# Kernel tuning notes

Hardware: AMD Instinct MI355X
Metric: run time of the kernel (lower is better)

Reference implementation:

```python
import jax, jax.numpy as jnp
import numpy as np

N_NODES = 20000
N_EDGES = 320000
IN_CH = 64
OUT_CH = 128

def _gat(x, src, dst, W, a_src, a_dst, bias, concat):
    # PyG GATConv: linear -> per-edge leaky_relu attention logits -> segment softmax over dst -> scatter-weighted sum
    N = x.shape[0]
    H, C = a_src.shape
    xl = (x @ W).reshape(N, H, C)                       # [N,H,C]
    al = (xl * a_src).sum(-1)                           # [N,H] src logits
    ar = (xl * a_dst).sum(-1)                           # [N,H] dst logits
    e = jax.nn.leaky_relu(al[src] + ar[dst], 0.2)       # [E,H]
    emax = jax.ops.segment_max(e, dst, num_segments=N)  # every node has a self loop -> no empty segments
    ee = jnp.exp(e - emax[dst])
    denom = jax.ops.segment_sum(ee, dst, num_segments=N)
    alpha = ee / (denom[dst] + 1e-16)                   # [E,H]
    out = jax.ops.segment_sum(xl[src] * alpha[:, :, None], dst, num_segments=N)  # [N,H,C]
    out = out.reshape(N, H * C) if concat else out.mean(axis=1)
    return out + bias

def setup_inputs() -> dict:
    key = jax.random.key(0)
    ks = jax.random.split(key, 32)
    def lin(k, fi, fo):
        return jax.random.normal(k, (fi, fo), jnp.float32) / np.sqrt(fi)
    def att(k, H, C):
        return jax.random.normal(k, (H, C), jnp.float32) / np.sqrt(C)
    x = jax.random.normal(ks[0], (N_NODES, IN_CH), jnp.float32)
    src = jax.random.randint(ks[1], (N_EDGES,), 0, N_NODES, jnp.int32)
    dst = jax.random.randint(ks[2], (N_EDGES,), 0, N_NODES, jnp.int32)
    dst = jnp.where(dst == src, (dst + 1) % N_NODES, dst)  # avoid pre-existing self loops
    edge_index = jnp.stack([src, dst])
    edge_time = jax.random.uniform(ks[3], (N_EDGES,), jnp.float32)
    H = 4
    return {
        "x": x, "edge_time": edge_time,
        "W1": lin(ks[4], IN_CH, 512), "as1": att(ks[5], H, 128), "ad1": att(ks[6], H, 128), "b1": jnp.zeros((512,), jnp.float32),
        "W2": lin(ks[7], 512, 512),   "as2": att(ks[8], H, 128), "ad2": att(ks[9], H, 128), "b2": jnp.zeros((512,), jnp.float32),
        "W3": lin(ks[10], 512, 512),  "as3": att(ks[11], H, 128), "ad3": att(ks[12], H, 128), "b3": jnp.zeros((OUT_CH,), jnp.float32),
        "tW1": lin(ks[13], 1, 64), "tb1": jnp.zeros((64,), jnp.float32),
        "tW2": lin(ks[14], 64, OUT_CH), "tb2": jnp.zeros((OUT_CH,), jnp.float32),
        "fW1": lin(ks[15], 2 * OUT_CH, OUT_CH), "fb1": jnp.zeros((OUT_CH,), jnp.float32),
        "fW2": lin(ks[16], OUT_CH, OUT_CH), "fb2": jnp.zeros((OUT_CH,), jnp.float32),
        "ln_g": jnp.ones((OUT_CH,), jnp.float32), "ln_b": jnp.zeros((OUT_CH,), jnp.float32),
        "rW": lin(ks[17], IN_CH, OUT_CH), "rb": jnp.zeros((OUT_CH,), jnp.float32),
        "edge_index": edge_index,
    }

def reference(x, edge_time, W1, as1, ad1, b1, W2, as2, ad2, b2, W3, as3, ad3, b3,
              tW1, tb1, tW2, tb2, fW1, fb1, fW2, fb2, ln_g, ln_b, rW, rb, edge_index):
    N = x.shape[0]
    loop = jnp.arange(N, dtype=edge_index.dtype)
    src = jnp.concatenate([edge_index[0], loop])
    dst = jnp.concatenate([edge_index[1], loop])
    # temporal embedding of raw (pre-self-loop) edges
    t = edge_time[:, None]
    time_emb = jax.nn.relu(t @ tW1 + tb1) @ tW2 + tb2    # [E, OUT_CH]
    x_res = x @ rW + rb
    h = jax.nn.relu(_gat(x, src, dst, W1, as1, ad1, b1, True))
    h = jax.nn.relu(_gat(h, src, dst, W2, as2, ad2, b2, True))
    h = jax.nn.relu(_gat(h, src, dst, W3, as3, ad3, b3, False))
    # x_agg[row] += h[col]  with (row, col) = (src, dst) incl. self loops
    agg = jax.ops.segment_sum(h[dst], src, num_segments=N)
    tm = jnp.broadcast_to(time_emb.mean(axis=0)[None, :], (N, time_emb.shape[1]))
    z = jnp.concatenate([agg, tm], axis=1)
    z = jax.nn.relu(z @ fW1 + fb1)                        # dropout is identity in eval
    z = z @ fW2 + fb2
    mu = z.mean(-1, keepdims=True)
    var = ((z - mu) ** 2).mean(-1, keepdims=True)
    z = (z - mu) / jnp.sqrt(var + 1e-5) * ln_g + ln_b
    return z + x_res
```

## Files before the change

### kernel.cpp

```cpp
#include <hip/hip_runtime.h>
#include <hip/hip_bf16.h>
#include <math.h>

typedef short bf16x8 __attribute__((ext_vector_type(8)));
typedef float f32x4 __attribute__((ext_vector_type(4)));

__device__ __forceinline__ float lrelu(float v) { return v > 0.f ? v : 0.2f * v; }

__device__ __forceinline__ void gload16(const void* g, void* l) {
  __builtin_amdgcn_global_load_lds(
      (const __attribute__((address_space(1))) void*)g,
      (__attribute__((address_space(3))) void*)l, 16, 0, 0);
}

__device__ __forceinline__ uint packbf(float v0, float v1) {
  __hip_bfloat16 h0 = __float2bfloat16(v0);
  __hip_bfloat16 h1 = __float2bfloat16(v1);
  return (uint)(*(unsigned short*)&h0) | ((uint)(*(unsigned short*)&h1) << 16);
}

__global__ void k_count(const int* __restrict__ src, const int* __restrict__ dst, int E,
                        int* cntD, int* cntS) {
  int e = blockIdx.x * blockDim.x + threadIdx.x;
  if (e < E) {
    atomicAdd(&cntD[dst[e]], 1);
    atomicAdd(&cntS[src[e]], 1);
  }
}

__global__ __launch_bounds__(1024) void k_scan2(const int* __restrict__ cntD, int* __restrict__ offD,
                                                const int* __restrict__ cntS, int* __restrict__ offS,
                                                int n) {
  const int* cnt = blockIdx.x ? cntS : cntD;
  int* off = blockIdx.x ? offS : offD;
  __shared__ int sums[1024];
  int t = threadIdx.x;
  int PT = (n + 1023) >> 10;
  int start = t * PT;
  int local = 0;
  for (int i = 0; i < PT; ++i) {
    int idx = start + i;
    if (idx < n) local += cnt[idx];
  }
  sums[t] = local;
  __syncthreads();
  for (int o = 1; o < 1024; o <<= 1) {
    int v = (t >= o) ? sums[t - o] : 0;
    __syncthreads();
    sums[t] += v;
    __syncthreads();
  }
  int run = sums[t] - local;
  for (int i = 0; i < PT; ++i) {
    int idx = start + i;
    if (idx < n) { off[idx] = run; run += cnt[idx]; }
  }
  if (t == 1023) off[n] = run;
}

__global__ void k_fill(const int* __restrict__ src, const int* __restrict__ dst, int E,
                       const int* __restrict__ offD, int* curD, int* lstD,
                       const int* __restrict__ offS, int* curS, int* lstS) {
  int e = blockIdx.x * blockDim.x + threadIdx.x;
  if (e < E) {
    int d = dst[e], s = src[e];
    int p = atomicAdd(&curD[d], 1);
    lstD[offD[d] + p] = s;
    int q = atomicAdd(&curS[s], 1);
    lstS[offS[s] + q] = d;
  }
}

__global__ __launch_bounds__(256) void k_time_reduce(const float* __restrict__ et,
    const float* __restrict__ tW1, const float* __restrict__ tb1,
    float* __restrict__ tacc, int E) {
  __shared__ float se[256];
  __shared__ float buf[256];
  int t = threadIdx.x;
  int l = t & 63, w = t >> 6;
  float wk = tW1[l], bk = tb1[l];
  float a0 = 0.f, a1 = 0.f, a2 = 0.f, a3 = 0.f;
  for (int base = blockIdx.x * 256; base < E; base += gridDim.x * 256) {
    int idx = base + t;
    se[t] = (idx < E) ? et[idx] : 0.f;
    __syncthreads();
    int cnt = E - base; if (cnt > 256) cnt = 256;
    int s0 = w * 64;
    int c = cnt - s0; if (c < 0) c = 0; if (c > 64) c = 64;
    int j = 0;
    for (; j + 4 <= c; j += 4) {
      float v0 = se[s0 + j], v1 = se[s0 + j + 1];
      float v2 = se[s0 + j + 2], v3 = se[s0 + j + 3];
      a0 += fmaxf(v0 * wk + bk, 0.f);
      a1 += fmaxf(v1 * wk + bk, 0.f);
      a2 += fmaxf(v2 * wk + bk, 0.f);
      a3 += fmaxf(v3 * wk + bk, 0.f);
    }
    for (; j < c; ++j) a0 += fmaxf(se[s0 + j] * wk + bk, 0.f);
    __syncthreads();
  }
  buf[t] = (a0 + a1) + (a2 + a3);
  __syncthreads();
  if (t < 64) {
    float s = buf[t] + buf[t + 64] + buf[t + 128] + buf[t + 192];
    atomicAdd(&tacc[t], s);
  }
}

__global__ __launch_bounds__(128) void k_time_combine(const float* __restrict__ tacc,
    const float* __restrict__ tW2, const float* __restrict__ tb2,
    const float* __restrict__ fW1, const float* __restrict__ fb1,
    float* __restrict__ cvec, int E) {
  __shared__ float tm[128];
  int t = threadIdx.x;
  float inv = 1.f / (float)E;
  float acc = tb2[t];
  for (int k = 0; k < 64; ++k) acc += (tacc[k] * inv) * tW2[k * 128 + t];
  tm[t] = acc;
  __syncthreads();
  float c = fb1[t];
  for (int k = 0; k < 128; ++k) c += tm[k] * fW1[(128 + k) * 128 + t];
  cvec[t] = c;
}

struct PrepArgs {
  const float* W[6]; __hip_bfloat16* Wt[6]; int K[6]; int Nw[6]; int tstart[6];
  int NC, XB;
};

__global__ __launch_bounds__(256) void k_prep(PrepArgs a, const float* __restrict__ x,
    __hip_bfloat16* __restrict__ xbf, __hip_bfloat16* __restrict__ habf,
    __hip_bfloat16* __restrict__ aggbf, int N, int Mp) {
  __shared__ float tile[32][65];
  int bid = blockIdx.x;
  int t = threadIdx.x;
  if (bid < a.NC) {
    int m = 0;
#pragma unroll
    for (int i = 1; i < 6; ++i) if (bid >= a.tstart[i]) m = i;
    const float* W = a.W[m];
    __hip_bfloat16* Wt = a.Wt[m];
    int K = a.K[m], Nw = a.Nw[m];
    int lt = bid - a.tstart[m];
    int ntn = Nw >> 6;
    int bk = (lt / ntn) * 32, bn = (lt % ntn) * 64;
    int rn = t & 63, rk = t >> 6;
#pragma unroll
    for (int i = 0; i < 8; ++i)
      tile[rk + i * 4][rn] = W[(size_t)(bk + rk + i * 4) * Nw + bn + rn];
    __syncthreads();
    int wk2 = (t & 15) * 2, wn = t >> 4;
    uint* Wo = (uint*)Wt;
#pragma unroll
    for (int i = 0; i < 4; ++i) {
      int n = wn + i * 16;
      Wo[((size_t)(bn + n) * K + bk + wk2) >> 1] = packbf(tile[wk2][n], tile[wk2 + 1][n]);
    }
  } else if (bid < a.NC + a.XB) {
    int i4 = (bid - a.NC) * 256 + t;
    int row = i4 >> 4;
    float4 v = make_float4(0.f, 0.f, 0.f, 0.f);
    if (row < N) v = ((const float4*)x)[i4];
    uint2 p; p.x = packbf(v.x, v.y); p.y = packbf(v.z, v.w);
    ((uint2*)xbf)[i4] = p;
  } else {
    int row = N + (bid - a.NC - a.XB);
    ((uint*)habf)[(size_t)row * 256 + t] = 0;
    if (t < 64) ((uint*)aggbf)[(size_t)row * 64 + t] = 0;
  }
}

template<int EPI>
__global__ __launch_bounds__(256) void gemm_t(
    const __hip_bfloat16* __restrict__ A, const __hip_bfloat16* __restrict__ Bt,
    void* __restrict__ Cout, const float* __restrict__ bias,
    int M, int Nw, int K, int relu, int Nn,
    const float* __restrict__ asrc, const float* __restrict__ adst,
    float* __restrict__ al, float* __restrict__ ar,
    float* __restrict__ C2, const float* __restrict__ bias2,
    const float* __restrict__ lng, const float* __restrict__ lnb,
    float* __restrict__ resid)
{
  __shared__ short As[128 * 32];
  __shared__ short Bs[128 * 32];
  int tid = threadIdx.x;
  int bm = blockIdx.x * 128;
  int cb = blockIdx.y;
  int bn = cb * 128;
  int w = tid >> 6, l = tid & 63;
  int wr = (w >> 1) * 64, wc = (w & 1) * 64;
  f32x4 acc[4][4] = {};
  const short* Ag = (const short*)A;
  const short* Bg = (const short*)Bt;

  for (int k0 = 0; k0 < K; k0 += 32) {
#pragma unroll
    for (int i = 0; i < 2; ++i) {
      int slot = i * 256 + tid;
      int row = slot >> 2;
      int col = (slot & 3) * 8;
      gload16(Ag + (size_t)(bm + row) * K + k0 + col, &As[slot * 8]);
      gload16(Bg + (size_t)(bn + row) * K + k0 + col, &Bs[slot * 8]);
    }
    __syncthreads();
    bf16x8 af[4], bfr[4];
#pragma unroll
    for (int m = 0; m < 4; ++m)
      af[m] = *(const bf16x8*)&As[(wr + m * 16 + (l & 15)) * 32 + (l >> 4) * 8];
#pragma unroll
    for (int n = 0; n < 4; ++n)
      bfr[n] = *(const bf16x8*)&Bs[(wc + n * 16 + (l & 15)) * 32 + (l >> 4) * 8];
#pragma unroll
    for (int m = 0; m < 4; ++m)
#pragma unroll
      for (int n = 0; n < 4; ++n)
        acc[m][n] = __builtin_amdgcn_mfma_f32_16x16x32_bf16(af[m], bfr[n], acc[m][n], 0, 0, 0);
    __syncthreads();
  }

  int g = l >> 4, cc = l & 15, cr = g * 4;

  if (EPI == 0) {
#pragma unroll
    for (int n = 0; n < 4; ++n) {
      int col = bn + wc + n * 16 + cc;
      float bb = bias ? bias[col] : 0.f;
#pragma unroll
      for (int m = 0; m < 4; ++m) {
#pragma unroll
        for (int r = 0; r < 4; ++r) {
          int gm = bm + wr + m * 16 + cr + r;
          if (gm < M) {
            float v = acc[m][n][r] + bb;
            if (relu) v = fmaxf(v, 0.f);
            ((__hip_bfloat16*)Cout)[(size_t)gm * Nw + col] = __float2bfloat16(v);
          }
        }
      }
    }
  }

  if (EPI == 1) {
    if (cb < 4) {
#pragma unroll
      for (int n = 0; n < 4; ++n) {
        int col = bn + wc + n * 16 + cc;
#pragma unroll
        for (int m = 0; m < 4; ++m) {
#pragma unroll
          for (int r = 0; r < 4; ++r) {
            int gm = bm + wr + m * 16 + cr + r;
            if (gm < M)
              ((__hip_bfloat16*)Cout)[(size_t)gm * 512 + col] = __float2bfloat16(acc[m][n][r]);
          }
        }
      }
      float asv[4], adv[4];
#pragma unroll
      for (int n = 0; n < 4; ++n) {
        int ch = bn + wc + n * 16 + cc;
        asv[n] = asrc[ch]; adv[n] = adst[ch];
      }
      float* spal = (float*)As;
      float* spar = spal + 256;
#pragma unroll
      for (int m = 0; m < 4; ++m) {
#pragma unroll
        for (int r = 0; r < 4; ++r) {
          float pa = acc[m][0][r] * asv[0] + acc[m][1][r] * asv[1]
                   + acc[m][2][r] * asv[2] + acc[m][3][r] * asv[3];
          float pb = acc[m][0][r] * adv[0] + acc[m][1][r] * adv[1]
                   + acc[m][2][r] * adv[2] + acc[m][3][r] * adv[3];
#pragma unroll
          for (int o = 1; o < 16; o <<= 1) {
            pa += __shfl_xor(pa, o);
            pb += __shfl_xor(pb, o);
          }
          if (cc == 0) {
            int rl = m * 16 + cr + r;
            spal[w * 64 + rl] = pa;
            spar[w * 64 + rl] = pb;
          }
        }
      }
      __syncthreads();
      if ((w & 1) == 0) {
        float av = spal[w * 64 + l] + spal[(w + 1) * 64 + l];
        float rv = spar[w * 64 + l] + spar[(w + 1) * 64 + l];
        int row = bm + wr + l;
        if (row < Nn) { al[row * 4 + cb] = av; ar[row * 4 + cb] = rv; }
      }
    } else {
#pragma unroll
      for (int n = 0; n < 4; ++n) {
        int col2 = wc + n * 16 + cc;
        float bb = bias2[col2];
#pragma unroll
        for (int m = 0; m < 4; ++m) {
#pragma unroll
          for (int r = 0; r < 4; ++r) {
            int gm = bm + wr + m * 16 + cr + r;
            if (gm < Nn) C2[(size_t)gm * 128 + col2] = acc[m][n][r] + bb;
          }
        }
      }
    }
  }

  if (EPI == 2) {
    float bb[4], gl_[4], gb_[4];
#pragma unroll
    for (int n = 0; n < 4; ++n) {
      int col = wc + n * 16 + cc;
      bb[n] = bias[col]; gl_[n] = lng[col]; gb_[n] = lnb[col];
    }
    float* ssum = (float*)As;
    float* ssq = ssum + 256;
    float* smu = ssum + 512;
    float* srs = ssum + 640;
#pragma unroll
    for (int m = 0; m < 4; ++m) {
#pragma unroll
      for (int r = 0; r < 4; ++r) {
        float s = 0.f, q = 0.f;
#pragma unroll
        for (int n = 0; n < 4; ++n) {
          float z = acc[m][n][r] + bb[n];
          s += z; q += z * z;
        }
#pragma unroll
        for (int o = 1; o < 16; o <<= 1) {
          s += __shfl_xor(s, o);
          q += __shfl_xor(q, o);
        }
        if (cc == 0) {
          int rl = m * 16 + cr + r;
          ssum[w * 64 + rl] = s;
          ssq[w * 64 + rl] = q;
        }
      }
    }
    __syncthreads();
    if ((w & 1) == 0) {
      float s = ssum[w * 64 + l] + ssum[(w + 1) * 64 + l];
      float q = ssq[w * 64 + l] + ssq[(w + 1) * 64 + l];
      float mu = s * (1.f / 128.f);
      float var = q * (1.f / 128.f) - mu * mu;
      smu[wr + l] = mu;
      srs[wr + l] = rsqrtf(var + 1e-5f);
    }
    __syncthreads();
#pragma unroll
    for (int m = 0; m < 4; ++m) {
#pragma unroll
      for (int r = 0; r < 4; ++r) {
        int rl = wr + m * 16 + cr + r;
        int gm = bm + rl;
        if (gm < M) {
          float mu = smu[rl], rs = srs[rl];
#pragma unroll
          for (int n = 0; n < 4; ++n) {
            int col = wc + n * 16 + cc;
            float z = acc[m][n][r] + bb[n];
            float y = (z - mu) * rs * gl_[n] + gb_[n] + resid[(size_t)gm * 128 + col];
            resid[(size_t)gm * 128 + col] = y;
          }
        }
      }
    }
  }
}

__global__ __launch_bounds__(256) void k_gat_agg(
    const __hip_bfloat16* __restrict__ xl, const float* __restrict__ al,
    const float* __restrict__ ar, const int* __restrict__ off,
    const int* __restrict__ lst, const float* __restrict__ bias,
    __hip_bfloat16* __restrict__ outb, __hip_bfloat16* __restrict__ outh,
    int mode, int N)
{
  __shared__ int   sside[4][64];
  __shared__ float sebuf[4][4][68];
  int w = threadIdx.x >> 6, l = threadIdx.x & 63;
  int d = blockIdx.x * 4 + w;
  bool active = (d < N);
  int base = 0, deg = 0, tot = 0;
  float4 arv = make_float4(0.f, 0.f, 0.f, 0.f);
  if (active) {
    base = off[d]; deg = off[d + 1] - base; tot = deg + 1;
    arv = *(const float4*)(ar + 4 * d);
  }
  int hh = l >> 4;
  float facc[8] = {0.f, 0.f, 0.f, 0.f, 0.f, 0.f, 0.f, 0.f};
  float dn0 = 0.f, dn1 = 0.f, dn2 = 0.f, dn3 = 0.f;
  const uint4* xw = (const uint4*)xl;
  for (int cb = 0; cb < tot; cb += 64) {
    int j = cb + l;
    float e0 = 0.f, e1 = 0.f, e2 = 0.f, e3 = 0.f;
    int sid = 0;
    if (j < tot) {
      sid = (j == deg) ? d : lst[base + j];
      float4 av = *(const float4*)(al + 4 * sid);
      e0 = __expf(lrelu(av.x + arv.x));
      e1 = __expf(lrelu(av.y + arv.y));
      e2 = __expf(lrelu(av.z + arv.z));
      e3 = __expf(lrelu(av.w + arv.w));
      dn0 += e0; dn1 += e1; dn2 += e2; dn3 += e3;
    }
    sside[w][l] = sid;
    sebuf[w][0][l] = e0; sebuf[w][1][l] = e1;
    sebuf[w][2][l] = e2; sebuf[w][3][l] = e3;
    int cnt = tot - cb; if (cnt > 64) cnt = 64;
#pragma unroll 2
    for (int jj = 0; jj < cnt; ++jj) {
      int sid2 = sside[w][jj];
      float e = sebuf[w][hh][jj];
      uint4 pv = xw[(size_t)sid2 * 64 + l];
      facc[0] += e * __uint_as_float(pv.x << 16);
      facc[1] += e * __uint_as_float(pv.x & 0xffff0000u);
      facc[2] += e * __uint_as_float(pv.y << 16);
      facc[3] += e * __uint_as_float(pv.y & 0xffff0000u);
      facc[4] += e * __uint_as_float(pv.z << 16);
      facc[5] += e * __uint_as_float(pv.z & 0xffff0000u);
      facc[6] += e * __uint_as_float(pv.w << 16);
      facc[7] += e * __uint_as_float(pv.w & 0xffff0000u);
    }
  }
#pragma unroll
  for (int o = 1; o < 64; o <<= 1) {
    dn0 += __shfl_xor(dn0, o); dn1 += __shfl_xor(dn1, o);
    dn2 += __shfl_xor(dn2, o); dn3 += __shfl_xor(dn3, o);
  }
  if (!active) return;
  float dsel = hh == 0 ? dn0 : hh == 1 ? dn1 : hh == 2 ? dn2 : dn3;
  float rden = 1.f / dsel;
  if (mode == 0) {
    int c8 = l * 8;
    const float4* bp = (const float4*)(bias + c8);
    float4 b0 = bp[0], b1 = bp[1];
    float vb[8] = {b0.x, b0.y, b0.z, b0.w, b1.x, b1.y, b1.z, b1.w};
    uint4 o4; uint* po = (uint*)&o4;
#pragma unroll
    for (int i = 0; i < 4; ++i) {
      float v0 = fmaxf(facc[2*i]   * rden + vb[2*i],   0.f);
      float v1 = fmaxf(facc[2*i+1] * rden + vb[2*i+1], 0.f);
      po[i] = packbf(v0, v1);
    }
    ((uint4*)outb)[(size_t)d * 64 + l] = o4;
  } else {
#pragma unroll
    for (int i = 0; i < 8; ++i) {
      facc[i] *= rden;
      facc[i] += __shfl_xor(facc[i], 16);
      facc[i] += __shfl_xor(facc[i], 32);
    }
    if (l < 16) {
      int c = l * 8;
      const float4* bp = (const float4*)(bias + c);
      float4 b0 = bp[0], b1 = bp[1];
      float vb[8] = {b0.x, b0.y, b0.z, b0.w, b1.x, b1.y, b1.z, b1.w};
      uint4 o4; uint* po = (uint*)&o4;
#pragma unroll
      for (int i = 0; i < 4; ++i) {
        float v0 = fmaxf(facc[2*i]   * 0.25f + vb[2*i],   0.f);
        float v1 = fmaxf(facc[2*i+1] * 0.25f + vb[2*i+1], 0.f);
        po[i] = packbf(v0, v1);
      }
      ((uint4*)outh)[(size_t)d * 16 + l] = o4;
    }
  }
}

__global__ __launch_bounds__(256) void k_aggsrc(const __hip_bfloat16* __restrict__ h3,
    const int* __restrict__ off, const int* __restrict__ lst,
    __hip_bfloat16* __restrict__ out, int N) {
  int w = threadIdx.x >> 6, l = threadIdx.x & 63;
  int n = blockIdx.x * 4 + w;
  if (n >= N) return;
  const uint* hw = (const uint*)h3;
  uint pv = hw[(size_t)n * 64 + l];
  float a0 = __uint_as_float(pv << 16);
  float a1 = __uint_as_float(pv & 0xffff0000u);
  float b0 = 0.f, b1 = 0.f;
  int b = off[n], e = off[n + 1];
  int j = b;
  for (; j + 2 <= e; j += 2) {
    int s0 = lst[j], s1 = lst[j + 1];
    uint q0 = hw[(size_t)s0 * 64 + l];
    uint q1 = hw[(size_t)s1 * 64 + l];
    a0 += __uint_as_float(q0 << 16);
    a1 += __uint_as_float(q0 & 0xffff0000u);
    b0 += __uint_as_float(q1 << 16);
    b1 += __uint_as_float(q1 & 0xffff0000u);
  }
  if (j < e) {
    uint q = hw[(size_t)lst[j] * 64 + l];
    a0 += __uint_as_float(q << 16);
    a1 += __uint_as_float(q & 0xffff0000u);
  }
  ((uint*)out)[(size_t)n * 64 + l] = packbf(a0 + b0, a1 + b1);
}

extern "C" void kernel_launch(void* const* d_in, const int* in_sizes, int n_in,
                              void* d_out, int out_size, void* d_ws, size_t ws_size,
                              hipStream_t stream) {
  (void)n_in; (void)out_size; (void)ws_size;
  const float* x   = (const float*)d_in[0];
  const float* et  = (const float*)d_in[1];
  const float* W1  = (const float*)d_in[2];
  const float* as1 = (const float*)d_in[3];
  const float* ad1 = (const float*)d_in[4];
  const float* b1  = (const float*)d_in[5];
  const float* W2  = (const float*)d_in[6];
  const float* as2 = (const float*)d_in[7];
  const float* ad2 = (const float*)d_in[8];
  const float* b2  = (const float*)d_in[9];
  const float* W3  = (const float*)d_in[10];
  const float* as3 = (const float*)d_in[11];
  const float* ad3 = (const float*)d_in[12];
  const float* b3  = (const float*)d_in[13];
  const float* tW1 = (const float*)d_in[14];
  const float* tb1 = (const float*)d_in[15];
  const float* tW2 = (const float*)d_in[16];
  const float* tb2 = (const float*)d_in[17];
  const float* fW1 = (const float*)d_in[18];
  const float* fb1 = (const float*)d_in[19];
  const float* fW2 = (const float*)d_in[20];
  const float* fb2 = (const float*)d_in[21];
  const float* lng = (const float*)d_in[22];
  const float* lnb = (const float*)d_in[23];
  const float* rW  = (const float*)d_in[24];
  const float* rb  = (const float*)d_in[25];
  const int*   ei  = (const int*)d_in[26];
  const int N = in_sizes[0] / 64;
  const int E = in_sizes[26] / 2;
  const int Mp = ((N + 127) / 128) * 128;
  const int* src = ei;
  const int* dst = ei + E;

  char* cur = (char*)d_ws;
  auto carve = [&](size_t bytes) { char* p = cur; cur += (bytes + 255) & ~(size_t)255; return p; };
  __hip_bfloat16* xbf  = (__hip_bfloat16*)carve((size_t)Mp * 64 * 2);
  __hip_bfloat16* habf = (__hip_bfloat16*)carve((size_t)Mp * 512 * 2);
  __hip_bfloat16* xlbf = (__hip_bfloat16*)carve((size_t)Mp * 512 * 2);
  __hip_bfloat16* wtCat= (__hip_bfloat16*)carve((size_t)640 * 64 * 2);
  __hip_bfloat16* wt2  = (__hip_bfloat16*)carve((size_t)512 * 512 * 2);
  __hip_bfloat16* wt3  = (__hip_bfloat16*)carve((size_t)512 * 512 * 2);
  __hip_bfloat16* wtF1 = (__hip_bfloat16*)carve((size_t)128 * 128 * 2);
  __hip_bfloat16* wtF2 = (__hip_bfloat16*)carve((size_t)128 * 128 * 2);
  __hip_bfloat16* aggbf= (__hip_bfloat16*)carve((size_t)Mp * 128 * 2);
  __hip_bfloat16* z1bf = (__hip_bfloat16*)carve((size_t)Mp * 128 * 2);
  __hip_bfloat16* h3   = (__hip_bfloat16*)carve((size_t)N * 128 * 2);
  float* al   = (float*)carve((size_t)N * 4 * 4);
  float* ar   = (float*)carve((size_t)N * 4 * 4);
  float* cvec = (float*)carve(128 * 4);
  int* offD = (int*)carve((size_t)(N + 1) * 4);
  int* offS = (int*)carve((size_t)(N + 1) * 4);
  int* lstD = (int*)carve((size_t)E * 4);
  int* lstS = (int*)carve((size_t)E * 4);
  char* zstart = cur;
  int* cntD = (int*)carve((size_t)N * 4);
  int* curD = (int*)carve((size_t)N * 4);
  int* cntS = (int*)carve((size_t)N * 4);
  int* curS = (int*)carve((size_t)N * 4);
  float* tacc = (float*)carve(64 * 4);
  size_t zbytes = (size_t)(cur - zstart);
  float* xres = (float*)d_out;

  hipMemsetAsync(zstart, 0, zbytes, stream);

  k_count<<<(E + 255) / 256, 256, 0, stream>>>(src, dst, E, cntD, cntS);
  k_scan2<<<2, 1024, 0, stream>>>(cntD, offD, cntS, offS, N);
  k_fill<<<(E + 255) / 256, 256, 0, stream>>>(src, dst, E, offD, curD, lstD, offS, curS, lstS);

  k_time_reduce<<<256, 256, 0, stream>>>(et, tW1, tb1, tacc, E);
  k_time_combine<<<1, 128, 0, stream>>>(tacc, tW2, tb2, fW1, fb1, cvec, E);

  {
    PrepArgs pa;
    int ts = 0;
    auto setd = [&](int i, const float* W, __hip_bfloat16* Wt, int K, int Nw) {
      pa.W[i] = W; pa.Wt[i] = Wt; pa.K[i] = K; pa.Nw[i] = Nw; pa.tstart[i] = ts;
      ts += (K / 32) * (Nw / 64);
    };
    setd(0, W1, wtCat, 64, 512);
    setd(1, W2, wt2, 512, 512);
    setd(2, W3, wt3, 512, 512);
    setd(3, rW, wtCat + (size_t)512 * 64, 64, 128);
    setd(4, fW1, wtF1, 128, 128);
    setd(5, fW2, wtF2, 128, 128);
    pa.NC = ts;
    pa.XB = Mp / 16;
    int grid = pa.NC + pa.XB + (Mp - N);
    k_prep<<<grid, 256, 0, stream>>>(pa, x, xbf, habf, aggbf, N, Mp);
  }

  const int TB = Mp / 128;
  const int GB = (N + 3) / 4;

  gemm_t<1><<<dim3(TB, 5), 256, 0, stream>>>(xbf, wtCat, xlbf, nullptr, Mp, 640, 64, 0, N,
      as1, ad1, al, ar, xres, rb, nullptr, nullptr, nullptr);
  k_gat_agg<<<GB, 256, 0, stream>>>(xlbf, al, ar, offD, lstD, b1, habf, nullptr, 0, N);
  gemm_t<1><<<dim3(TB, 4), 256, 0, stream>>>(habf, wt2, xlbf, nullptr, Mp, 512, 512, 0, N,
      as2, ad2, al, ar, nullptr, nullptr, nullptr, nullptr, nullptr);
  k_gat_agg<<<GB, 256, 0, stream>>>(xlbf, al, ar, offD, lstD, b2, habf, nullptr, 0, N);
  gemm_t<1><<<dim3(TB, 4), 256, 0, stream>>>(habf, wt3, xlbf, nullptr, Mp, 512, 512, 0, N,
      as3, ad3, al, ar, nullptr, nullptr, nullptr, nullptr, nullptr);
  k_gat_agg<<<GB, 256, 0, stream>>>(xlbf, al, ar, offD, lstD, b3, nullptr, h3, 1, N);

  k_aggsrc<<<GB, 256, 0, stream>>>(h3, offS, lstS, aggbf, N);

  gemm_t<0><<<dim3(TB, 1), 256, 0, stream>>>(aggbf, wtF1, z1bf, cvec, Mp, 128, 128, 1, N,
      nullptr, nullptr, nullptr, nullptr, nullptr, nullptr, nullptr, nullptr, nullptr);
  gemm_t<2><<<dim3(TB, 1), 256, 0, stream>>>(z1bf, wtF2, nullptr, fb2, N, 128, 128, 0, N,
      nullptr, nullptr, nullptr, nullptr, nullptr, nullptr, lng, lnb, xres);
}
```

Baseline: 407.0 us.

## Fuse time-embedding reduction into count/scan kernels, widen GEMM K-step, unroll gathers

Folds the time-embedding reduction into the edge-count kernel and the time-combine step into the scan kernel as an extra block, which removes two kernel launches. The GEMM now loads two 32-wide K slices per barrier, halving the number of synchronisations at the cost of doubling LDS use per block. The GAT aggregation and source-aggregation gather loops are unrolled by four to keep more independent loads in flight. The extra LDS and registers may lower occupancy.

```diff
diff --git a/kernel.cpp b/kernel.cpp
--- a/kernel.cpp
+++ b/kernel.cpp
@@ -19,22 +19,73 @@
   return (uint)(*(unsigned short*)&h0) | ((uint)(*(unsigned short*)&h1) << 16);
 }
 
-__global__ void k_count(const int* __restrict__ src, const int* __restrict__ dst, int E,
-                        int* cntD, int* cntS) {
-  int e = blockIdx.x * blockDim.x + threadIdx.x;
+__global__ __launch_bounds__(256) void k_countT(const int* __restrict__ src,
+    const int* __restrict__ dst, int E, int* cntD, int* cntS,
+    const float* __restrict__ et, const float* __restrict__ tW1,
+    const float* __restrict__ tb1, float* __restrict__ tacc) {
+  int t = threadIdx.x;
+  int e = blockIdx.x * 256 + t;
   if (e < E) {
     atomicAdd(&cntD[dst[e]], 1);
     atomicAdd(&cntS[src[e]], 1);
   }
-}
-
-__global__ __launch_bounds__(1024) void k_scan2(const int* __restrict__ cntD, int* __restrict__ offD,
-                                                const int* __restrict__ cntS, int* __restrict__ offS,
-                                                int n) {
+  if (blockIdx.x < 256) {
+    __shared__ float se[256];
+    __shared__ float buf[256];
+    int l = t & 63, w = t >> 6;
+    float wk = tW1[l], bk = tb1[l];
+    float a0 = 0.f, a1 = 0.f, a2 = 0.f, a3 = 0.f;
+    for (int base = blockIdx.x * 256; base < E; base += 256 * 256) {
+      int idx = base + t;
+      se[t] = (idx < E) ? et[idx] : 0.f;
+      __syncthreads();
+      int cnt = E - base; if (cnt > 256) cnt = 256;
+      int s0 = w * 64;
+      int c = cnt - s0; if (c < 0) c = 0; if (c > 64) c = 64;
+      int j = 0;
+      for (; j + 4 <= c; j += 4) {
+        a0 += fmaxf(se[s0 + j] * wk + bk, 0.f);
+        a1 += fmaxf(se[s0 + j + 1] * wk + bk, 0.f);
+        a2 += fmaxf(se[s0 + j + 2] * wk + bk, 0.f);
+        a3 += fmaxf(se[s0 + j + 3] * wk + bk, 0.f);
+      }
+      for (; j < c; ++j) a0 += fmaxf(se[s0 + j] * wk + bk, 0.f);
+      __syncthreads();
+    }
+    buf[t] = (a0 + a1) + (a2 + a3);
+    __syncthreads();
+    if (t < 64) {
+      float s = buf[t] + buf[t + 64] + buf[t + 128] + buf[t + 192];
+      atomicAdd(&tacc[t], s);
+    }
+  }
+}
+
+__global__ __launch_bounds__(1024) void k_scan2c(const int* __restrict__ cntD, int* __restrict__ offD,
+    const int* __restrict__ cntS, int* __restrict__ offS, int n,
+    const float* __restrict__ tacc, const float* __restrict__ tW2,
+    const float* __restrict__ tb2, const float* __restrict__ fW1,
+    const float* __restrict__ fb1, float* __restrict__ cvec, int E) {
+  int t = threadIdx.x;
+  if (blockIdx.x == 2) {
+    __shared__ float tm[128];
+    if (t < 128) {
+      float inv = 1.f / (float)E;
+      float acc = tb2[t];
+      for (int k = 0; k < 64; ++k) acc += (tacc[k] * inv) * tW2[k * 128 + t];
+      tm[t] = acc;
+    }
+    __syncthreads();
+    if (t < 128) {
+      float c = fb1[t];
+      for (int k = 0; k < 128; ++k) c += tm[k] * fW1[(128 + k) * 128 + t];
+      cvec[t] = c;
+    }
+    return;
+  }
   const int* cnt = blockIdx.x ? cntS : cntD;
   int* off = blockIdx.x ? offS : offD;
   __shared__ int sums[1024];
-  int t = threadIdx.x;
   int PT = (n + 1023) >> 10;
   int start = t * PT;
   int local = 0;
@@ -69,58 +120,6 @@
     int q = atomicAdd(&curS[s], 1);
     lstS[offS[s] + q] = d;
   }
-}
-
-__global__ __launch_bounds__(256) void k_time_reduce(const float* __restrict__ et,
-    const float* __restrict__ tW1, const float* __restrict__ tb1,
-    float* __restrict__ tacc, int E) {
-  __shared__ float se[256];
-  __shared__ float buf[256];
-  int t = threadIdx.x;
-  int l = t & 63, w = t >> 6;
-  float wk = tW1[l], bk = tb1[l];
-  float a0 = 0.f, a1 = 0.f, a2 = 0.f, a3 = 0.f;
-  for (int base = blockIdx.x * 256; base < E; base += gridDim.x * 256) {
-    int idx = base + t;
-    se[t] = (idx < E) ? et[idx] : 0.f;
-    __syncthreads();
-    int cnt = E - base; if (cnt > 256) cnt = 256;
-    int s0 = w * 64;
-    int c = cnt - s0; if (c < 0) c = 0; if (c > 64) c = 64;
-    int j = 0;
-    for (; j + 4 <= c; j += 4) {
-      float v0 = se[s0 + j], v1 = se[s0 + j + 1];
-      float v2 = se[s0 + j + 2], v3 = se[s0 + j + 3];
-      a0 += fmaxf(v0 * wk + bk, 0.f);
-      a1 += fmaxf(v1 * wk + bk, 0.f);
-      a2 += fmaxf(v2 * wk + bk, 0.f);
-      a3 += fmaxf(v3 * wk + bk, 0.f);
-    }
-    for (; j < c; ++j) a0 += fmaxf(se[s0 + j] * wk + bk, 0.f);
-    __syncthreads();
-  }
-  buf[t] = (a0 + a1) + (a2 + a3);
-  __syncthreads();
-  if (t < 64) {
-    float s = buf[t] + buf[t + 64] + buf[t + 128] + buf[t + 192];
-    atomicAdd(&tacc[t], s);
-  }
-}
-
-__global__ __launch_bounds__(128) void k_time_combine(const float* __restrict__ tacc,
-    const float* __restrict__ tW2, const float* __restrict__ tb2,
-    const float* __restrict__ fW1, const float* __restrict__ fb1,
-    float* __restrict__ cvec, int E) {
-  __shared__ float tm[128];
-  int t = threadIdx.x;
-  float inv = 1.f / (float)E;
-  float acc = tb2[t];
-  for (int k = 0; k < 64; ++k) acc += (tacc[k] * inv) * tW2[k * 128 + t];
-  tm[t] = acc;
-  __syncthreads();
-  float c = fb1[t];
-  for (int k = 0; k < 128; ++k) c += tm[k] * fW1[(128 + k) * 128 + t];
-  cvec[t] = c;
 }
 
 struct PrepArgs {
@@ -181,8 +180,10 @@
     const float* __restrict__ lng, const float* __restrict__ lnb,
     float* __restrict__ resid)
 {
-  __shared__ short As[128 * 32];
-  __shared__ short Bs[128 * 32];
+  __shared__ short As0[128 * 32];
+  __shared__ short As1[128 * 32];
+  __shared__ short Bs0[128 * 32];
+  __shared__ short Bs1[128 * 32];
   int tid = threadIdx.x;
   int bm = blockIdx.x * 128;
   int cb = blockIdx.y;
@@ -193,28 +194,48 @@
   const short* Ag = (const short*)A;
   const short* Bg = (const short*)Bt;
 
-  for (int k0 = 0; k0 < K; k0 += 32) {
+  for (int k0 = 0; k0 < K; k0 += 64) {
 #pragma unroll
     for (int i = 0; i < 2; ++i) {
       int slot = i * 256 + tid;
       int row = slot >> 2;
       int col = (slot & 3) * 8;
-      gload16(Ag + (size_t)(bm + row) * K + k0 + col, &As[slot * 8]);
-      gload16(Bg + (size_t)(bn + row) * K + k0 + col, &Bs[slot * 8]);
-    }
-    __syncthreads();
-    bf16x8 af[4], bfr[4];
-#pragma unroll
-    for (int m = 0; m < 4; ++m)
-      af[m] = *(const bf16x8*)&As[(wr + m * 16 + (l & 15)) * 32 + (l >> 4) * 8];
-#pragma unroll
-    for (int n = 0; n < 4; ++n)
-      bfr[n] = *(const bf16x8*)&Bs[(wc + n * 16 + (l & 15)) * 32 + (l >> 4) * 8];
-#pragma unroll
-    for (int m = 0; m < 4; ++m)
+      const short* Arow = Ag + (size_t)(bm + row) * K + k0 + col;
+      const short* Brow = Bg + (size_t)(bn + row) * K + k0 + col;
+      gload16(Arow, &As0[slot * 8]);
+      gload16(Arow + 32, &As1[slot * 8]);
+      gload16(Brow, &Bs0[slot * 8]);
+      gload16(Brow + 32, &Bs1[slot * 8]);
+    }
+    __syncthreads();
+    {
+      bf16x8 af[4], bfr[4];
+#pragma unroll
+      for (int m = 0; m < 4; ++m)
+        af[m] = *(const bf16x8*)&As0[(wr + m * 16 + (l & 15)) * 32 + (l >> 4) * 8];
 #pragma unroll
       for (int n = 0; n < 4; ++n)
-        acc[m][n] = __builtin_amdgcn_mfma_f32_16x16x32_bf16(af[m], bfr[n], acc[m][n], 0, 0, 0);
+        bfr[n] = *(const bf16x8*)&Bs0[(wc + n * 16 + (l & 15)) * 32 + (l >> 4) * 8];
+#pragma unroll
+      for (int m = 0; m < 4; ++m)
+#pragma unroll
+        for (int n = 0; n < 4; ++n)
+          acc[m][n] = __builtin_amdgcn_mfma_f32_16x16x32_bf16(af[m], bfr[n], acc[m][n], 0, 0, 0);
+    }
+    {
+      bf16x8 af[4], bfr[4];
+#pragma unroll
+      for (int m = 0; m < 4; ++m)
+        af[m] = *(const bf16x8*)&As1[(wr + m * 16 + (l & 15)) * 32 + (l >> 4) * 8];
+#pragma unroll
+      for (int n = 0; n < 4; ++n)
+        bfr[n] = *(const bf16x8*)&Bs1[(wc + n * 16 + (l & 15)) * 32 + (l >> 4) * 8];
+#pragma unroll
+      for (int m = 0; m < 4; ++m)
+#pragma unroll
+        for (int n = 0; n < 4; ++n)
+          acc[m][n] = __builtin_amdgcn_mfma_f32_16x16x32_bf16(af[m], bfr[n], acc[m][n], 0, 0, 0);
+    }
     __syncthreads();
   }
 
@@ -261,7 +282,7 @@
         int ch = bn + wc + n * 16 + cc;
         asv[n] = asrc[ch]; adv[n] = adst[ch];
       }
-      float* spal = (float*)As;
+      float* spal = (float*)As0;
       float* spar = spal + 256;
 #pragma unroll
       for (int m = 0; m < 4; ++m) {
@@ -314,7 +335,7 @@
       int col = wc + n * 16 + cc;
       bb[n] = bias[col]; gl_[n] = lng[col]; gb_[n] = lnb[col];
     }
-    float* ssum = (float*)As;
+    float* ssum = (float*)As0;
     float* ssq = ssum + 256;
     float* smu = ssum + 512;
     float* srs = ssum + 640;
@@ -393,6 +414,16 @@
   float facc[8] = {0.f, 0.f, 0.f, 0.f, 0.f, 0.f, 0.f, 0.f};
   float dn0 = 0.f, dn1 = 0.f, dn2 = 0.f, dn3 = 0.f;
   const uint4* xw = (const uint4*)xl;
+  auto fma8 = [&](uint4 pv, float e) {
+    facc[0] += e * __uint_as_float(pv.x << 16);
+    facc[1] += e * __uint_as_float(pv.x & 0xffff0000u);
+    facc[2] += e * __uint_as_float(pv.y << 16);
+    facc[3] += e * __uint_as_float(pv.y & 0xffff0000u);
+    facc[4] += e * __uint_as_float(pv.z << 16);
+    facc[5] += e * __uint_as_float(pv.z & 0xffff0000u);
+    facc[6] += e * __uint_as_float(pv.w << 16);
+    facc[7] += e * __uint_as_float(pv.w & 0xffff0000u);
+  };
   for (int cb = 0; cb < tot; cb += 64) {
     int j = cb + l;
     float e0 = 0.f, e1 = 0.f, e2 = 0.f, e3 = 0.f;
@@ -410,19 +441,23 @@
     sebuf[w][0][l] = e0; sebuf[w][1][l] = e1;
     sebuf[w][2][l] = e2; sebuf[w][3][l] = e3;
     int cnt = tot - cb; if (cnt > 64) cnt = 64;
-#pragma unroll 2
-    for (int jj = 0; jj < cnt; ++jj) {
-      int sid2 = sside[w][jj];
-      float e = sebuf[w][hh][jj];
-      uint4 pv = xw[(size_t)sid2 * 64 + l];
-      facc[0] += e * __uint_as_float(pv.x << 16);
-      facc[1] += e * __uint_as_float(pv.x & 0xffff0000u);
-      facc[2] += e * __uint_as_float(pv.y << 16);
-      facc[3] += e * __uint_as_float(pv.y & 0xffff0000u);
-      facc[4] += e * __uint_as_float(pv.z << 16);
-      facc[5] += e * __uint_as_float(pv.z & 0xffff0000u);
-      facc[6] += e * __uint_as_float(pv.w << 16);
-      facc[7] += e * __uint_as_float(pv.w & 0xffff0000u);
+    int jj = 0;
+    for (; jj + 4 <= cnt; jj += 4) {
+      int s0 = sside[w][jj], s1 = sside[w][jj + 1];
+      int s2 = sside[w][jj + 2], s3 = sside[w][jj + 3];
+      float ea = sebuf[w][hh][jj], eb = sebuf[w][hh][jj + 1];
+      float ec = sebuf[w][hh][jj + 2], ed = sebuf[w][hh][jj + 3];
+      uint4 p0 = xw[(size_t)s0 * 64 + l];
+      uint4 p1 = xw[(size_t)s1 * 64 + l];
+      uint4 p2 = xw[(size_t)s2 * 64 + l];
+      uint4 p3 = xw[(size_t)s3 * 64 + l];
+      fma8(p0, ea); fma8(p1, eb); fma8(p2, ec); fma8(p3, ed);
+    }
+    for (; jj < cnt; ++jj) {
+      int s0 = sside[w][jj];
+      float ea = sebuf[w][hh][jj];
+      uint4 p0 = xw[(size_t)s0 * 64 + l];
+      fma8(p0, ea);
     }
   }
 #pragma unroll
@@ -480,24 +515,26 @@
   uint pv = hw[(size_t)n * 64 + l];
   float a0 = __uint_as_float(pv << 16);
   float a1 = __uint_as_float(pv & 0xffff0000u);
-  float b0 = 0.f, b1 = 0.f;
+  float b0 = 0.f, b1 = 0.f, c0 = 0.f, c1 = 0.f, d0 = 0.f, d1 = 0.f;
   int b = off[n], e = off[n + 1];
   int j = b;
-  for (; j + 2 <= e; j += 2) {
-    int s0 = lst[j], s1 = lst[j + 1];
+  for (; j + 4 <= e; j += 4) {
+    int s0 = lst[j], s1 = lst[j + 1], s2 = lst[j + 2], s3 = lst[j + 3];
     uint q0 = hw[(size_t)s0 * 64 + l];
     uint q1 = hw[(size_t)s1 * 64 + l];
-    a0 += __uint_as_float(q0 << 16);
-    a1 += __uint_as_float(q0 & 0xffff0000u);
-    b0 += __uint_as_float(q1 << 16);
-    b1 += __uint_as_float(q1 & 0xffff0000u);
-  }
-  if (j < e) {
+    uint q2 = hw[(size_t)s2 * 64 + l];
+    uint q3 = hw[(size_t)s3 * 64 + l];
+    a0 += __uint_as_float(q0 << 16); a1 += __uint_as_float(q0 & 0xffff0000u);
+    b0 += __uint_as_float(q1 << 16); b1 += __uint_as_float(q1 & 0xffff0000u);
+    c0 += __uint_as_float(q2 << 16); c1 += __uint_as_float(q2 & 0xffff0000u);
+    d0 += __uint_as_float(q3 << 16); d1 += __uint_as_float(q3 & 0xffff0000u);
+  }
+  for (; j < e; ++j) {
     uint q = hw[(size_t)lst[j] * 64 + l];
     a0 += __uint_as_float(q << 16);
     a1 += __uint_as_float(q & 0xffff0000u);
   }
-  ((uint*)out)[(size_t)n * 64 + l] = packbf(a0 + b0, a1 + b1);
+  ((uint*)out)[(size_t)n * 64 + l] = packbf((a0 + b0) + (c0 + d0), (a1 + b1) + (c1 + d1));
 }
 
 extern "C" void kernel_launch(void* const* d_in, const int* in_sizes, int n_in,
@@ -568,12 +605,9 @@
 
   hipMemsetAsync(zstart, 0, zbytes, stream);
 
-  k_count<<<(E + 255) / 256, 256, 0, stream>>>(src, dst, E, cntD, cntS);
-  k_scan2<<<2, 1024, 0, stream>>>(cntD, offD, cntS, offS, N);
+  k_countT<<<(E + 255) / 256, 256, 0, stream>>>(src, dst, E, cntD, cntS, et, tW1, tb1, tacc);
+  k_scan2c<<<3, 1024, 0, stream>>>(cntD, offD, cntS, offS, N, tacc, tW2, tb2, fW1, fb1, cvec, E);
   k_fill<<<(E + 255) / 256, 256, 0, stream>>>(src, dst, E, offD, curD, lstD, offS, curS, lstS);
-
-  k_time_reduce<<<256, 256, 0, stream>>>(et, tW1, tb1, tacc, E);
-  k_time_combine<<<1, 128, 0, stream>>>(tacc, tW2, tb2, fW1, fb1, cvec, E);
 
   {
     PrepArgs pa;
```

After: 380.4 us. -6.5%, faster.
